# Kernel tuning notes

Hardware: AMD Instinct MI355X
Metric: run time of the kernel (lower is better)

## Reference

```python
import jax, jax.numpy as jnp
import numpy as np

N_NODES = 50000


def _gcn_norm(edge_index, num_nodes):
    # add self loops, compute symmetric normalization D^-1/2 (A+I) D^-1/2
    loops = jnp.arange(num_nodes, dtype=edge_index.dtype)
    row = jnp.concatenate([edge_index[0], loops])
    col = jnp.concatenate([edge_index[1], loops])
    deg = jax.ops.segment_sum(jnp.ones_like(row, dtype=jnp.float32), col,
                              num_segments=num_nodes)
    dinv = jnp.where(deg > 0, jax.lax.rsqrt(deg), 0.0)
    norm = dinv[row] * dinv[col]  # [E']
    return row, col, norm


def _gcn_conv(x, W, b, row, col, norm, num_nodes):
    h = x @ W                       # [N, out] transform first (smaller dim)
    msg = h[row] * norm[:, None]    # gather along source nodes  [E', out]
    agg = jax.ops.segment_sum(msg, col, num_segments=num_nodes)  # scatter-add
    return agg + b


def setup_inputs() -> dict:
    key = jax.random.key(0)
    k1, k2, k3, k4 = jax.random.split(key, 4)
    x = jax.random.normal(k1, (N_NODES, 128), dtype=jnp.float32)
    edge_index = jax.random.randint(k2, (2, 800000), 0, N_NODES, dtype=jnp.int64)
    W1 = jax.random.normal(k3, (128, 128), dtype=jnp.float32) * (1.0 / np.sqrt(128))
    b1 = jnp.zeros((128,), dtype=jnp.float32)
    W2 = jax.random.normal(k4, (128, 16), dtype=jnp.float32) * (1.0 / np.sqrt(128))
    b2 = jnp.zeros((16,), dtype=jnp.float32)
    return {"x": x, "edge_index": edge_index, "W1": W1, "b1": b1, "W2": W2, "b2": b2}


def reference(x, edge_index, W1, b1, W2, b2):
    n = x.shape[0]
    row, col, norm = _gcn_norm(edge_index, n)
    h = _gcn_conv(x, W1, b1, row, col, norm, n)
    h = jax.nn.relu(h)
    h = _gcn_conv(h, W2, b2, row, col, norm, n)
    return jax.nn.log_softmax(h, axis=1)
```

## Files before the change

kernel.cpp:

```cpp
#include <hip/hip_runtime.h>
#include <math.h>

constexpr int N  = 50000;
constexpr int E  = 800000;
constexpr int F1 = 128;
constexpr int F2 = 16;
constexpr int BSHIFT  = 8;
constexpr int NBUCKET = (N + 255) >> BSHIFT;
constexpr int CHUNK   = 2048;
constexpr int CAP     = 6144;
constexpr int SBLK    = (E + CHUNK - 1) / CHUNK;
constexpr int GBLK    = 391;
constexpr int CSTRIDE = 32;

typedef unsigned short ushort_t;
typedef unsigned char  uchar_t;
typedef __bf16 bf16x8 __attribute__((ext_vector_type(8)));
typedef float  f32x4  __attribute__((ext_vector_type(4)));

static __device__ __forceinline__ float blo(unsigned u) { return __uint_as_float(u << 16); }
static __device__ __forceinline__ float bhi(unsigned u) { return __uint_as_float(u & 0xffff0000u); }
static __device__ __forceinline__ ushort_t to_bf(float f) { __bf16 h = (__bf16)f; return *(ushort_t*)&h; }
static __device__ __forceinline__ uchar_t to_fp8(float f) {
    return (uchar_t)(__builtin_amdgcn_cvt_pk_fp8_f32(f, f, 0, false) & 0xff);
}
template <int S>
static __device__ __forceinline__ float cf8(unsigned u) {
    return __builtin_amdgcn_cvt_f32_fp8(u, S);
}

__global__ __launch_bounds__(256) void k_scatterP_gemm1(const int* __restrict__ row,
                                                        const int* __restrict__ col,
                                                        int* __restrict__ cursor,
                                                        unsigned* __restrict__ P,
                                                        const float* __restrict__ x,
                                                        const float* __restrict__ W1,
                                                        uchar_t* __restrict__ h1q) {
    __shared__ __align__(16) ushort_t Wl[F1 * 136];
    int t = threadIdx.x;

    if (blockIdx.x < SBLK) {
        int* hist = (int*)Wl;
        int* loff = hist + 256;
        int* gst  = loff + 256;
        int* lcur = gst + 256;
        int* wtot = lcur + 256;
        unsigned* eb  = (unsigned*)(wtot + 8);
        uchar_t*  bbk = (uchar_t*)(eb + 2048);
        int base = blockIdx.x * CHUNK;
        int total = min(CHUNK, E - base);
        hist[t] = 0;
        __syncthreads();
        int ce[CHUNK / 256];
#pragma unroll
        for (int i = 0; i < CHUNK / 256; ++i) {
            int e = base + i * 256 + t;
            ce[i] = (e < E) ? col[e] : -1;
            if (ce[i] >= 0) atomicAdd(&hist[ce[i] >> BSHIFT], 1);
        }
        __syncthreads();
        {
            int lane = t & 63, wid = t >> 6;
            int v = hist[t];
            int incl = v;
#pragma unroll
            for (int d = 1; d < 64; d <<= 1) {
                int u = __shfl_up(incl, d, 64);
                if (lane >= d) incl += u;
            }
            if (lane == 63) wtot[wid] = incl;
            __syncthreads();
            int wb = 0;
            for (int w = 0; w < wid; ++w) wb += wtot[w];
            int ex = wb + incl - v;
            loff[t] = ex;
            lcur[t] = ex;
            if (t < NBUCKET) gst[t] = t * CAP + atomicAdd(&cursor[t * CSTRIDE], v);
        }
        __syncthreads();
#pragma unroll
        for (int i = 0; i < CHUNK / 256; ++i) {
            int e = base + i * 256 + t;
            if (ce[i] >= 0) {
                int b = ce[i] >> BSHIFT;
                int pos = atomicAdd(&lcur[b], 1);
                eb[pos]  = ((unsigned)row[e] << BSHIFT) | (unsigned)(ce[i] & 255);
                bbk[pos] = (uchar_t)b;
            }
        }
        __syncthreads();
#pragma unroll
        for (int i = 0; i < CHUNK / 256; ++i) {
            int k = i * 256 + t;
            if (k < total) {
                int b = bbk[k];
                P[gst[b] + (k - loff[b])] = eb[k];
            }
        }
        return;
    }

    int gb = blockIdx.x - SBLK;
    {
        int n = t & 127, kh = t >> 7;
#pragma unroll
        for (int j = 0; j < 8; ++j) {
            int k0 = (kh * 8 + j) * 8;
            bf16x8 w;
#pragma unroll
            for (int i2 = 0; i2 < 8; ++i2) w[i2] = (__bf16)W1[(k0 + i2) * F1 + n];
            *(bf16x8*)&Wl[n * 136 + k0] = w;
        }
    }
    __syncthreads();

    int lane = t & 63, wv = t >> 6;
    int quad = lane >> 4, l15 = lane & 15;
#pragma unroll 1
    for (int tile = gb * 2; tile < gb * 2 + 2; ++tile) {
        int arow = tile * 64 + wv * 16 + l15;
        int rclamp = min(arow, N - 1);
        f32x4 acc[8] = {};
#pragma unroll
        for (int kk = 0; kk < 4; ++kk) {
            int k0 = kk * 32 + quad * 8;
            const float* xp = x + (size_t)rclamp * F1 + k0;
            float4 u0 = *(const float4*)xp;
            float4 u1 = *(const float4*)(xp + 4);
            bf16x8 a;
            a[0] = (__bf16)u0.x; a[1] = (__bf16)u0.y; a[2] = (__bf16)u0.z; a[3] = (__bf16)u0.w;
            a[4] = (__bf16)u1.x; a[5] = (__bf16)u1.y; a[6] = (__bf16)u1.z; a[7] = (__bf16)u1.w;
#pragma unroll
            for (int ct = 0; ct < 8; ++ct) {
                bf16x8 b = *(const bf16x8*)&Wl[(ct * 16 + l15) * 136 + k0];
                acc[ct] = __builtin_amdgcn_mfma_f32_16x16x32_bf16(a, b, acc[ct], 0, 0, 0);
            }
        }
        int orow0 = tile * 64 + wv * 16 + quad * 4;
#pragma unroll
        for (int r = 0; r < 4; ++r) {
            int orow = orow0 + r;
            if (orow < N) {
#pragma unroll
                for (int ct = 0; ct < 8; ++ct)
                    h1q[(size_t)orow * F1 + ct * 16 + l15] = to_fp8(acc[ct][r]);
            }
        }
    }
}

__global__ __launch_bounds__(1024) void k_binFinal(const unsigned* __restrict__ P,
                                                   const int* __restrict__ cursor,
                                                   ushort_t* __restrict__ csr16,
                                                   int* __restrict__ seg_start,
                                                   int* __restrict__ counts,
                                                   float* __restrict__ dinv) {
    __shared__ unsigned eb[CAP];
    __shared__ int cnt[256];
    __shared__ int cur[256];
    __shared__ int wtot[4];
    int t = threadIdx.x;
    int b = blockIdx.x;
    int lo = b << BSHIFT;
    int n_nodes = min(256, N - lo);
    int m = cursor[b * CSTRIDE];
    if (t < 256) cnt[t] = 0;
    __syncthreads();
    const unsigned* Pb = P + (size_t)b * CAP;
    for (int k = t; k < m; k += 1024) {
        unsigned u = Pb[k];
        eb[k] = u;
        atomicAdd(&cnt[u & 255], 1);
    }
    __syncthreads();
    int lane = t & 63, wid = t >> 6;
    int v = 0, incl = 0;
    if (t < 256) {
        v = cnt[t];
        incl = v;
#pragma unroll
        for (int d = 1; d < 64; d <<= 1) {
            int u = __shfl_up(incl, d, 64);
            if (lane >= d) incl += u;
        }
        if (lane == 63) wtot[wid] = incl;
    }
    __syncthreads();
    if (t < 256) {
        int wb = 0;
        for (int w = 0; w < wid; ++w) wb += wtot[w];
        int o = b * CAP + wb + incl - v;
        cur[t] = o;
        if (t < n_nodes) {
            seg_start[lo + t] = o;
            counts[lo + t] = v;
            dinv[lo + t] = rsqrtf((float)v + 1.f);
        }
    }
    __syncthreads();
    for (int k = t; k < m; k += 1024) {
        unsigned u = eb[k];
        int pos = atomicAdd(&cur[u & 255], 1);
        csr16[pos] = (ushort_t)(u >> BSHIFT);
    }
}

__global__ __launch_bounds__(256) void k_gather1_gemm2(const uchar_t* __restrict__ h1q,
                                                       const int* __restrict__ seg_start,
                                                       const int* __restrict__ counts,
                                                       const ushort_t* __restrict__ csr16,
                                                       const float* __restrict__ dinv,
                                                       const float* __restrict__ W2,
                                                       const float* __restrict__ b1,
                                                       ushort_t* __restrict__ h2s) {
    __shared__ __align__(16) ushort_t W2l[F2 * 136];
    __shared__ __align__(16) ushort_t T[16 * 136];
    __shared__ float dv[16];
    int t = threadIdx.x;
    for (int i = t; i < F1 * F2; i += 256) {
        int k = i >> 4, n = i & 15;
        W2l[n * 136 + k] = to_bf(W2[i]);
    }
    int lane = t & 63, wv = t >> 6;
    int g = lane >> 4, l15 = lane & 15;
    int gbase = lane & 48;
    int nl = wv * 4 + g;
    int c = blockIdx.x * 16 + nl;
    int cl = min(c, N - 1);

    float dc = 0.f;
    int s = seg_start[cl];
    int cnt = 0;
    if (c < N) { dc = dinv[c]; cnt = counts[c]; }
    uint2 wsf = *(const uint2*)(h1q + ((size_t)cl << 7) + (l15 << 3));
    float4 bL = ((const float4*)b1)[l15 * 2];
    float4 bH = ((const float4*)b1)[l15 * 2 + 1];
    int mcnt = cnt;
    mcnt = max(mcnt, __shfl_xor(mcnt, 16));
    mcnt = max(mcnt, __shfl_xor(mcnt, 32));

    float a0 = 0.f, a1 = 0.f, a2 = 0.f, a3 = 0.f;
    float a4 = 0.f, a5 = 0.f, a6 = 0.f, a7 = 0.f;

#define G1FLT(j_, jb_) { unsigned u = __shfl(pk, gbase + (jb_) + (j_));                     \
        e##j_ = __uint_as_float(u & 0xffff0000u);                                           \
        w##j_ = *(const uint2*)(h1q + ((size_t)(u & 0xffffu) << 7) + (l15 << 3)); }
#define G1ACC(j_) {                                                                         \
        a0 = fmaf(e##j_, cf8<0>(w##j_.x), a0); a1 = fmaf(e##j_, cf8<1>(w##j_.x), a1);       \
        a2 = fmaf(e##j_, cf8<2>(w##j_.x), a2); a3 = fmaf(e##j_, cf8<3>(w##j_.x), a3);       \
        a4 = fmaf(e##j_, cf8<0>(w##j_.y), a4); a5 = fmaf(e##j_, cf8<1>(w##j_.y), a5);       \
        a6 = fmaf(e##j_, cf8<2>(w##j_.y), a6); a7 = fmaf(e##j_, cf8<3>(w##j_.y), a7); }

    unsigned pk = 0;
    {   int k = l15;
        if (k < cnt) {
            int r = csr16[s + k];
            pk = ((unsigned)to_bf(dinv[r]) << 16) | (unsigned)r;
        }
    }
#pragma unroll 1
    for (int k0 = 0; k0 < mcnt; k0 += 16) {
        unsigned pknext = 0;
        {   int k = k0 + 16 + l15;
            if (k < cnt) {
                int r = csr16[s + k];
                pknext = ((unsigned)to_bf(dinv[r]) << 16) | (unsigned)r;
            }
        }
        {
            uint2 w0, w1, w2, w3, w4, w5, w6, w7;
            float e0, e1, e2, e3, e4, e5, e6, e7;
            G1FLT(0, 0) G1FLT(1, 0) G1FLT(2, 0) G1FLT(3, 0)
            G1FLT(4, 0) G1FLT(5, 0) G1FLT(6, 0) G1FLT(7, 0)
            G1ACC(0) G1ACC(1) G1ACC(2) G1ACC(3)
            G1ACC(4) G1ACC(5) G1ACC(6) G1ACC(7)
        }
        if (k0 + 8 < mcnt) {
            uint2 w0, w1, w2, w3, w4, w5, w6, w7;
            float e0, e1, e2, e3, e4, e5, e6, e7;
            G1FLT(0, 8) G1FLT(1, 8) G1FLT(2, 8) G1FLT(3, 8)
            G1FLT(4, 8) G1FLT(5, 8) G1FLT(6, 8) G1FLT(7, 8)
            G1ACC(0) G1ACC(1) G1ACC(2) G1ACC(3)
            G1ACC(4) G1ACC(5) G1ACC(6) G1ACC(7)
        }
        pk = pknext;
    }
#undef G1FLT
#undef G1ACC

    {
        a0 = fmaf(dc, cf8<0>(wsf.x), a0); a1 = fmaf(dc, cf8<1>(wsf.x), a1);
        a2 = fmaf(dc, cf8<2>(wsf.x), a2); a3 = fmaf(dc, cf8<3>(wsf.x), a3);
        a4 = fmaf(dc, cf8<0>(wsf.y), a4); a5 = fmaf(dc, cf8<1>(wsf.y), a5);
        a6 = fmaf(dc, cf8<2>(wsf.y), a6); a7 = fmaf(dc, cf8<3>(wsf.y), a7);
        a0 = fmaxf(fmaf(dc, a0, bL.x), 0.f); a1 = fmaxf(fmaf(dc, a1, bL.y), 0.f);
        a2 = fmaxf(fmaf(dc, a2, bL.z), 0.f); a3 = fmaxf(fmaf(dc, a3, bL.w), 0.f);
        a4 = fmaxf(fmaf(dc, a4, bH.x), 0.f); a5 = fmaxf(fmaf(dc, a5, bH.y), 0.f);
        a6 = fmaxf(fmaf(dc, a6, bH.z), 0.f); a7 = fmaxf(fmaf(dc, a7, bH.w), 0.f);
        uint4 pp;
        pp.x = (unsigned)to_bf(a0) | ((unsigned)to_bf(a1) << 16);
        pp.y = (unsigned)to_bf(a2) | ((unsigned)to_bf(a3) << 16);
        pp.z = (unsigned)to_bf(a4) | ((unsigned)to_bf(a5) << 16);
        pp.w = (unsigned)to_bf(a6) | ((unsigned)to_bf(a7) << 16);
        *(uint4*)&T[nl * 136 + (l15 << 3)] = pp;
        if (l15 == 0) dv[nl] = dc;
    }
    __syncthreads();

    if (wv == 0) {
        int quad = lane >> 4;
        f32x4 acc = {};
#pragma unroll
        for (int kk = 0; kk < 4; ++kk) {
            int k0 = kk * 32 + quad * 8;
            bf16x8 a = *(const bf16x8*)&T[l15 * 136 + k0];
            bf16x8 b = *(const bf16x8*)&W2l[l15 * 136 + k0];
            acc = __builtin_amdgcn_mfma_f32_16x16x32_bf16(a, b, acc, 0, 0, 0);
        }
#pragma unroll
        for (int r = 0; r < 4; ++r) {
            int rw = quad * 4 + r;
            int gn = blockIdx.x * 16 + rw;
            if (gn < N) h2s[(size_t)gn * F2 + l15] = to_bf(acc[r] * dv[rw]);
        }
    }
}

__global__ __launch_bounds__(256) void k_gather2(const ushort_t* __restrict__ h2s,
                                                 const int* __restrict__ seg_start,
                                                 const int* __restrict__ counts,
                                                 const ushort_t* __restrict__ csr16,
                                                 const float* __restrict__ dinv,
                                                 const float* __restrict__ b2,
                                                 float* __restrict__ out) {
    int idx = blockIdx.x * 256 + threadIdx.x;
    int node = idx >> 3, sub = idx & 7;
    if (node >= N) return;
    int lane = threadIdx.x & 63;
    int gb = lane & 56;
    int s = seg_start[node], cntc = counts[node];
    float dc = dinv[node];
    float2 bb = ((const float2*)b2)[sub];
    unsigned us = ((const unsigned*)(h2s + (size_t)node * F2))[sub];
    float ax = 0.f, ay = 0.f;

#define G2LOAD(n_) { int src = gb | min(n_, rem - 1); int r = __shfl(rl, src);              \
        w##n_ = ((const unsigned*)(h2s + (size_t)r * F2))[sub]; if (n_ >= rem) w##n_ = 0u; }

    int rl = 0;
    if (sub < min(cntc, 8)) rl = csr16[s + sub];
#pragma unroll 1
    for (int j0 = 0; j0 < cntc; j0 += 8) {
        int rem = min(cntc - j0, 8);
        int rlnext = 0;
        int j2 = j0 + 8;
        if (j2 < cntc && sub < cntc - j2) rlnext = csr16[s + j2 + sub];
        unsigned w0, w1, w2, w3, w4, w5, w6, w7;
        G2LOAD(0) G2LOAD(1) G2LOAD(2) G2LOAD(3)
        G2LOAD(4) G2LOAD(5) G2LOAD(6) G2LOAD(7)
        ax += ((blo(w0) + blo(w1)) + (blo(w2) + blo(w3))) +
              ((blo(w4) + blo(w5)) + (blo(w6) + blo(w7)));
        ay += ((bhi(w0) + bhi(w1)) + (bhi(w2) + bhi(w3))) +
              ((bhi(w4) + bhi(w5)) + (bhi(w6) + bhi(w7)));
        rl = rlnext;
    }
#undef G2LOAD
    ax += blo(us);
    ay += bhi(us);
    float v0 = fmaf(dc, ax, bb.x);
    float v1 = fmaf(dc, ay, bb.y);
    float mx = fmaxf(v0, v1);
#pragma unroll
    for (int m = 1; m < 8; m <<= 1) mx = fmaxf(mx, __shfl_xor(mx, m));
    float sm = expf(v0 - mx) + expf(v1 - mx);
#pragma unroll
    for (int m = 1; m < 8; m <<= 1) sm += __shfl_xor(sm, m);
    float lse = mx + logf(sm);
    float2 o;
    o.x = v0 - lse;
    o.y = v1 - lse;
    ((float2*)(out + (size_t)node * F2))[sub] = o;
}

extern "C" void kernel_launch(void* const* d_in, const int* in_sizes, int n_in,
                              void* d_out, int out_size, void* d_ws, size_t ws_size,
                              hipStream_t stream) {
    const float* x  = (const float*)d_in[0];
    const int*   ei = (const int*)d_in[1];
    const float* W1 = (const float*)d_in[2];
    const float* b1 = (const float*)d_in[3];
    const float* W2 = (const float*)d_in[4];
    const float* b2 = (const float*)d_in[5];
    const int* row = ei;
    const int* col = ei + E;

    char* ws = (char*)d_ws;
    int*      cursor    = (int*)ws;      ws += 256 * CSTRIDE * 4;
    unsigned* P         = (unsigned*)ws; ws += (size_t)NBUCKET * CAP * 4;
    ushort_t* csr16     = (ushort_t*)ws; ws += (size_t)NBUCKET * CAP * 2;
    int*      seg_start = (int*)ws;      ws += (size_t)N * 4;
    int*      counts    = (int*)ws;      ws += (size_t)N * 4;
    float*    dinv      = (float*)ws;    ws += (size_t)N * 4;
    uchar_t*  h1q       = (uchar_t*)ws;  ws += (size_t)N * F1;
    ushort_t* h2s       = (ushort_t*)ws; ws += (size_t)N * F2 * 2;

    (void)hipMemsetAsync(cursor, 0, 256 * CSTRIDE * 4, stream);

    k_scatterP_gemm1<<<SBLK + GBLK, 256, 0, stream>>>(row, col, cursor, P, x, W1, h1q);
    k_binFinal<<<NBUCKET, 1024, 0, stream>>>(P, cursor, csr16, seg_start, counts, dinv);
    k_gather1_gemm2<<<(N + 15) / 16, 256, 0, stream>>>(h1q, seg_start, counts, csr16,
                                                       dinv, W2, b1, h2s);
    k_gather2<<<((size_t)N * 8 + 255) / 256, 256, 0, stream>>>(h2s, seg_start, counts, csr16,
                                                               dinv, b2, (float*)d_out);
}
```

Baseline: 142.7 us.

## Fuse all four stages into one cooperative persistent kernel with grid syncs

Replaces the memset and four separate launches with a single cooperative kernel sized from occupancy, using grid.sync between the scatter/GEMM1, bucket-finalize, gather1/GEMM2 and gather2 phases. The bucket scatter no longer uses global atomic cursors. Each chunk writes its locally sorted edges plus per-bucket counts and offsets, and the finalize phase rebuilds each bucket with a scan and a binary search. This removes launch gaps and global atomics, but adds grid-wide barriers and a persistent-loop schedule that may underuse the GPU in some phases, since finalize runs on only 196 blocks.

```diff
diff --git a/kernel.cpp b/kernel.cpp
--- a/kernel.cpp
+++ b/kernel.cpp
@@ -1,5 +1,8 @@
 #include <hip/hip_runtime.h>
+#include <hip/hip_cooperative_groups.h>
 #include <math.h>
+
+namespace cg = cooperative_groups;
 
 constexpr int N  = 50000;
 constexpr int E  = 800000;
@@ -10,8 +13,8 @@
 constexpr int CHUNK   = 2048;
 constexpr int CAP     = 6144;
 constexpr int SBLK    = (E + CHUNK - 1) / CHUNK;
-constexpr int GBLK    = 391;
-constexpr int CSTRIDE = 32;
+constexpr int TILES   = (N + 63) / 64;
+constexpr int GTILES  = (N + 15) / 16;
 
 typedef unsigned short ushort_t;
 typedef unsigned char  uchar_t;
@@ -29,218 +32,202 @@
     return __builtin_amdgcn_cvt_f32_fp8(u, S);
 }
 
-__global__ __launch_bounds__(256) void k_scatterP_gemm1(const int* __restrict__ row,
-                                                        const int* __restrict__ col,
-                                                        int* __restrict__ cursor,
-                                                        unsigned* __restrict__ P,
-                                                        const float* __restrict__ x,
-                                                        const float* __restrict__ W1,
-                                                        uchar_t* __restrict__ h1q) {
-    __shared__ __align__(16) ushort_t Wl[F1 * 136];
+static __device__ __forceinline__ int excl_scan256(int v, int* wtot, int& tot) {
     int t = threadIdx.x;
-
-    if (blockIdx.x < SBLK) {
-        int* hist = (int*)Wl;
+    int lane = t & 63, wid = t >> 6;
+    int incl = v;
+#pragma unroll
+    for (int d = 1; d < 64; d <<= 1) {
+        int u = __shfl_up(incl, d, 64);
+        if (lane >= d) incl += u;
+    }
+    if (lane == 63) wtot[wid] = incl;
+    __syncthreads();
+    int wb = 0;
+    for (int w = 0; w < wid; ++w) wb += wtot[w];
+    tot = wtot[0] + wtot[1] + wtot[2] + wtot[3];
+    __syncthreads();
+    return wb + incl - v;
+}
+
+__global__ __launch_bounds__(256, 4) void k_mega(
+    const int* __restrict__ row, const int* __restrict__ col,
+    const float* __restrict__ x, const float* __restrict__ W1,
+    const float* __restrict__ b1, const float* __restrict__ W2,
+    const float* __restrict__ b2,
+    unsigned* __restrict__ P2, int* __restrict__ cnt_g, int* __restrict__ loff_g,
+    ushort_t* __restrict__ csr16, int* __restrict__ seg_start,
+    int* __restrict__ counts, float* __restrict__ dinv,
+    uchar_t* __restrict__ h1q, ushort_t* __restrict__ h2s,
+    float* __restrict__ out)
+{
+    __shared__ __align__(16) char smem[35072];
+    cg::grid_group grid = cg::this_grid();
+    int t   = threadIdx.x;
+    int NBk = (int)gridDim.x;
+
+    int SC = min(SBLK, max(1, (NBk * 2) / 5));
+    if ((int)blockIdx.x < SC) {
+        int* hist = (int*)smem;
         int* loff = hist + 256;
-        int* gst  = loff + 256;
-        int* lcur = gst + 256;
+        int* lcur = loff + 256;
         int* wtot = lcur + 256;
-        unsigned* eb  = (unsigned*)(wtot + 8);
-        uchar_t*  bbk = (uchar_t*)(eb + 2048);
-        int base = blockIdx.x * CHUNK;
-        int total = min(CHUNK, E - base);
-        hist[t] = 0;
-        __syncthreads();
-        int ce[CHUNK / 256];
-#pragma unroll
-        for (int i = 0; i < CHUNK / 256; ++i) {
-            int e = base + i * 256 + t;
-            ce[i] = (e < E) ? col[e] : -1;
-            if (ce[i] >= 0) atomicAdd(&hist[ce[i] >> BSHIFT], 1);
-        }
-        __syncthreads();
-        {
-            int lane = t & 63, wid = t >> 6;
-            int v = hist[t];
-            int incl = v;
-#pragma unroll
-            for (int d = 1; d < 64; d <<= 1) {
-                int u = __shfl_up(incl, d, 64);
-                if (lane >= d) incl += u;
-            }
-            if (lane == 63) wtot[wid] = incl;
-            __syncthreads();
-            int wb = 0;
-            for (int w = 0; w < wid; ++w) wb += wtot[w];
-            int ex = wb + incl - v;
+        unsigned* eb = (unsigned*)(wtot + 8);
+        for (int j = blockIdx.x; j < SBLK; j += SC) {
+            hist[t] = 0;
+            __syncthreads();
+            int base = j * CHUNK;
+            int ce[CHUNK / 256];
+#pragma unroll
+            for (int i = 0; i < CHUNK / 256; ++i) {
+                int e = base + i * 256 + t;
+                ce[i] = (e < E) ? col[e] : -1;
+                if (ce[i] >= 0) atomicAdd(&hist[ce[i] >> BSHIFT], 1);
+            }
+            __syncthreads();
+            int tot;
+            int ex = excl_scan256(hist[t], wtot, tot);
             loff[t] = ex;
             lcur[t] = ex;
-            if (t < NBUCKET) gst[t] = t * CAP + atomicAdd(&cursor[t * CSTRIDE], v);
+            if (t < NBUCKET) { cnt_g[t * SBLK + j] = hist[t]; loff_g[t * SBLK + j] = ex; }
+            __syncthreads();
+#pragma unroll
+            for (int i = 0; i < CHUNK / 256; ++i) {
+                int e = base + i * 256 + t;
+                if (ce[i] >= 0) {
+                    int pos = atomicAdd(&lcur[ce[i] >> BSHIFT], 1);
+                    eb[pos] = ((unsigned)row[e] << BSHIFT) | (unsigned)(ce[i] & 255);
+                }
+            }
+            __syncthreads();
+            int total = min(CHUNK, E - base);
+#pragma unroll
+            for (int i = 0; i < CHUNK / 256; ++i) {
+                int k = i * 256 + t;
+                if (k < total) P2[base + k] = eb[k];
+            }
+            __syncthreads();
+        }
+    } else {
+        ushort_t* Wl = (ushort_t*)smem;
+        {
+            int n = t & 127, kh = t >> 7;
+#pragma unroll
+            for (int j = 0; j < 8; ++j) {
+                int k0 = (kh * 8 + j) * 8;
+                bf16x8 w;
+#pragma unroll
+                for (int i2 = 0; i2 < 8; ++i2) w[i2] = (__bf16)W1[(k0 + i2) * F1 + n];
+                *(bf16x8*)&Wl[n * 136 + k0] = w;
+            }
         }
         __syncthreads();
-#pragma unroll
-        for (int i = 0; i < CHUNK / 256; ++i) {
-            int e = base + i * 256 + t;
-            if (ce[i] >= 0) {
-                int b = ce[i] >> BSHIFT;
-                int pos = atomicAdd(&lcur[b], 1);
-                eb[pos]  = ((unsigned)row[e] << BSHIFT) | (unsigned)(ce[i] & 255);
-                bbk[pos] = (uchar_t)b;
-            }
-        }
+        int lane = t & 63, wv = t >> 6;
+        int quad = lane >> 4, l15 = lane & 15;
+        int gcount = NBk - SC;
+#pragma unroll 1
+        for (int tile = (int)blockIdx.x - SC; tile < TILES; tile += gcount) {
+            int arow = tile * 64 + wv * 16 + l15;
+            int rclamp = min(arow, N - 1);
+            f32x4 acc[8] = {};
+#pragma unroll
+            for (int kk = 0; kk < 4; ++kk) {
+                int k0 = kk * 32 + quad * 8;
+                const float* xp = x + (size_t)rclamp * F1 + k0;
+                float4 u0 = *(const float4*)xp;
+                float4 u1 = *(const float4*)(xp + 4);
+                bf16x8 a;
+                a[0] = (__bf16)u0.x; a[1] = (__bf16)u0.y; a[2] = (__bf16)u0.z; a[3] = (__bf16)u0.w;
+                a[4] = (__bf16)u1.x; a[5] = (__bf16)u1.y; a[6] = (__bf16)u1.z; a[7] = (__bf16)u1.w;
+#pragma unroll
+                for (int ct = 0; ct < 8; ++ct) {
+                    bf16x8 bfr = *(const bf16x8*)&Wl[(ct * 16 + l15) * 136 + k0];
+                    acc[ct] = __builtin_amdgcn_mfma_f32_16x16x32_bf16(a, bfr, acc[ct], 0, 0, 0);
+                }
+            }
+            int orow0 = tile * 64 + wv * 16 + quad * 4;
+#pragma unroll
+            for (int r = 0; r < 4; ++r) {
+                int orow = orow0 + r;
+                if (orow < N) {
+#pragma unroll
+                    for (int ct = 0; ct < 8; ++ct)
+                        h1q[(size_t)orow * F1 + ct * 16 + l15] = to_fp8(acc[ct][r]);
+                }
+            }
+        }
+    }
+    __threadfence();
+    grid.sync();
+
+    if ((int)blockIdx.x < NBUCKET) {
+        int b = blockIdx.x;
+        int* cS    = (int*)smem;
+        int* oS    = cS + SBLK;
+        int* baseS = oS + SBLK;
+        int* wtot2 = baseS + 392;
+        int* cnt   = wtot2 + 8;
+        int* cur   = cnt + 256;
+        unsigned* eb2 = (unsigned*)(cur + 256);
+        for (int jj = t; jj < SBLK; jj += 256) {
+            cS[jj] = cnt_g[b * SBLK + jj];
+            oS[jj] = loff_g[b * SBLK + jj];
+        }
+        cnt[t] = 0;
         __syncthreads();
-#pragma unroll
-        for (int i = 0; i < CHUNK / 256; ++i) {
-            int k = i * 256 + t;
-            if (k < total) {
-                int b = bbk[k];
-                P[gst[b] + (k - loff[b])] = eb[k];
-            }
-        }
-        return;
-    }
-
-    int gb = blockIdx.x - SBLK;
+        int tot0 = 0, tot1 = 0;
+        int e0 = excl_scan256(cS[t], wtot2, tot0);
+        baseS[t] = e0;
+        int v1 = (256 + t < SBLK) ? cS[256 + t] : 0;
+        int e1 = excl_scan256(v1, wtot2, tot1);
+        if (256 + t < SBLK) baseS[256 + t] = tot0 + e1;
+        int m = tot0 + tot1;
+        __syncthreads();
+        for (int k = t; k < m; k += 256) {
+            int lo2 = 0, hi2 = SBLK - 1;
+            while (lo2 < hi2) {
+                int mid = (lo2 + hi2 + 1) >> 1;
+                if (baseS[mid] <= k) lo2 = mid; else hi2 = mid - 1;
+            }
+            unsigned u = P2[lo2 * CHUNK + oS[lo2] + (k - baseS[lo2])];
+            eb2[k] = u;
+            atomicAdd(&cnt[u & 255], 1);
+        }
+        __syncthreads();
+        int tot2;
+        int exn = excl_scan256(cnt[t], wtot2, tot2);
+        int o = b * CAP + exn;
+        cur[t] = o;
+        int lo = b << BSHIFT;
+        int myc = cnt[t];
+        if (lo + t < N) {
+            seg_start[lo + t] = o;
+            counts[lo + t]    = myc;
+            dinv[lo + t]      = rsqrtf((float)myc + 1.f);
+        }
+        __syncthreads();
+        for (int k = t; k < m; k += 256) {
+            unsigned u = eb2[k];
+            int pos = atomicAdd(&cur[u & 255], 1);
+            csr16[pos] = (ushort_t)(u >> BSHIFT);
+        }
+    }
+    __threadfence();
+    grid.sync();
+
     {
-        int n = t & 127, kh = t >> 7;
-#pragma unroll
-        for (int j = 0; j < 8; ++j) {
-            int k0 = (kh * 8 + j) * 8;
-            bf16x8 w;
-#pragma unroll
-            for (int i2 = 0; i2 < 8; ++i2) w[i2] = (__bf16)W1[(k0 + i2) * F1 + n];
-            *(bf16x8*)&Wl[n * 136 + k0] = w;
-        }
-    }
-    __syncthreads();
-
-    int lane = t & 63, wv = t >> 6;
-    int quad = lane >> 4, l15 = lane & 15;
-#pragma unroll 1
-    for (int tile = gb * 2; tile < gb * 2 + 2; ++tile) {
-        int arow = tile * 64 + wv * 16 + l15;
-        int rclamp = min(arow, N - 1);
-        f32x4 acc[8] = {};
-#pragma unroll
-        for (int kk = 0; kk < 4; ++kk) {
-            int k0 = kk * 32 + quad * 8;
-            const float* xp = x + (size_t)rclamp * F1 + k0;
-            float4 u0 = *(const float4*)xp;
-            float4 u1 = *(const float4*)(xp + 4);
-            bf16x8 a;
-            a[0] = (__bf16)u0.x; a[1] = (__bf16)u0.y; a[2] = (__bf16)u0.z; a[3] = (__bf16)u0.w;
-            a[4] = (__bf16)u1.x; a[5] = (__bf16)u1.y; a[6] = (__bf16)u1.z; a[7] = (__bf16)u1.w;
-#pragma unroll
-            for (int ct = 0; ct < 8; ++ct) {
-                bf16x8 b = *(const bf16x8*)&Wl[(ct * 16 + l15) * 136 + k0];
-                acc[ct] = __builtin_amdgcn_mfma_f32_16x16x32_bf16(a, b, acc[ct], 0, 0, 0);
-            }
-        }
-        int orow0 = tile * 64 + wv * 16 + quad * 4;
-#pragma unroll
-        for (int r = 0; r < 4; ++r) {
-            int orow = orow0 + r;
-            if (orow < N) {
-#pragma unroll
-                for (int ct = 0; ct < 8; ++ct)
-                    h1q[(size_t)orow * F1 + ct * 16 + l15] = to_fp8(acc[ct][r]);
-            }
-        }
-    }
-}
-
-__global__ __launch_bounds__(1024) void k_binFinal(const unsigned* __restrict__ P,
-                                                   const int* __restrict__ cursor,
-                                                   ushort_t* __restrict__ csr16,
-                                                   int* __restrict__ seg_start,
-                                                   int* __restrict__ counts,
-                                                   float* __restrict__ dinv) {
-    __shared__ unsigned eb[CAP];
-    __shared__ int cnt[256];
-    __shared__ int cur[256];
-    __shared__ int wtot[4];
-    int t = threadIdx.x;
-    int b = blockIdx.x;
-    int lo = b << BSHIFT;
-    int n_nodes = min(256, N - lo);
-    int m = cursor[b * CSTRIDE];
-    if (t < 256) cnt[t] = 0;
-    __syncthreads();
-    const unsigned* Pb = P + (size_t)b * CAP;
-    for (int k = t; k < m; k += 1024) {
-        unsigned u = Pb[k];
-        eb[k] = u;
-        atomicAdd(&cnt[u & 255], 1);
-    }
-    __syncthreads();
-    int lane = t & 63, wid = t >> 6;
-    int v = 0, incl = 0;
-    if (t < 256) {
-        v = cnt[t];
-        incl = v;
-#pragma unroll
-        for (int d = 1; d < 64; d <<= 1) {
-            int u = __shfl_up(incl, d, 64);
-            if (lane >= d) incl += u;
-        }
-        if (lane == 63) wtot[wid] = incl;
-    }
-    __syncthreads();
-    if (t < 256) {
-        int wb = 0;
-        for (int w = 0; w < wid; ++w) wb += wtot[w];
-        int o = b * CAP + wb + incl - v;
-        cur[t] = o;
-        if (t < n_nodes) {
-            seg_start[lo + t] = o;
-            counts[lo + t] = v;
-            dinv[lo + t] = rsqrtf((float)v + 1.f);
-        }
-    }
-    __syncthreads();
-    for (int k = t; k < m; k += 1024) {
-        unsigned u = eb[k];
-        int pos = atomicAdd(&cur[u & 255], 1);
-        csr16[pos] = (ushort_t)(u >> BSHIFT);
-    }
-}
-
-__global__ __launch_bounds__(256) void k_gather1_gemm2(const uchar_t* __restrict__ h1q,
-                                                       const int* __restrict__ seg_start,
-                                                       const int* __restrict__ counts,
-                                                       const ushort_t* __restrict__ csr16,
-                                                       const float* __restrict__ dinv,
-                                                       const float* __restrict__ W2,
-                                                       const float* __restrict__ b1,
-                                                       ushort_t* __restrict__ h2s) {
-    __shared__ __align__(16) ushort_t W2l[F2 * 136];
-    __shared__ __align__(16) ushort_t T[16 * 136];
-    __shared__ float dv[16];
-    int t = threadIdx.x;
-    for (int i = t; i < F1 * F2; i += 256) {
-        int k = i >> 4, n = i & 15;
-        W2l[n * 136 + k] = to_bf(W2[i]);
-    }
-    int lane = t & 63, wv = t >> 6;
-    int g = lane >> 4, l15 = lane & 15;
-    int gbase = lane & 48;
-    int nl = wv * 4 + g;
-    int c = blockIdx.x * 16 + nl;
-    int cl = min(c, N - 1);
-
-    float dc = 0.f;
-    int s = seg_start[cl];
-    int cnt = 0;
-    if (c < N) { dc = dinv[c]; cnt = counts[c]; }
-    uint2 wsf = *(const uint2*)(h1q + ((size_t)cl << 7) + (l15 << 3));
-    float4 bL = ((const float4*)b1)[l15 * 2];
-    float4 bH = ((const float4*)b1)[l15 * 2 + 1];
-    int mcnt = cnt;
-    mcnt = max(mcnt, __shfl_xor(mcnt, 16));
-    mcnt = max(mcnt, __shfl_xor(mcnt, 32));
-
-    float a0 = 0.f, a1 = 0.f, a2 = 0.f, a3 = 0.f;
-    float a4 = 0.f, a5 = 0.f, a6 = 0.f, a7 = 0.f;
+        ushort_t* W2l = (ushort_t*)smem;
+        ushort_t* T   = W2l + F2 * 136;
+        float*    dv  = (float*)(T + 16 * 136);
+        for (int i = t; i < F1 * F2; i += 256) {
+            int k = i >> 4, n = i & 15;
+            W2l[n * 136 + k] = to_bf(W2[i]);
+        }
+        int lane = t & 63, wv = t >> 6;
+        int g = lane >> 4, l15 = lane & 15;
+        int gbase = lane & 48;
+        float4 bL = ((const float4*)b1)[l15 * 2];
+        float4 bH = ((const float4*)b1)[l15 * 2 + 1];
 
 #define G1FLT(j_, jb_) { unsigned u = __shfl(pk, gbase + (jb_) + (j_));                     \
         e##j_ = __uint_as_float(u & 0xffff0000u);                                           \
@@ -251,135 +238,151 @@
         a4 = fmaf(e##j_, cf8<0>(w##j_.y), a4); a5 = fmaf(e##j_, cf8<1>(w##j_.y), a5);       \
         a6 = fmaf(e##j_, cf8<2>(w##j_.y), a6); a7 = fmaf(e##j_, cf8<3>(w##j_.y), a7); }
 
-    unsigned pk = 0;
-    {   int k = l15;
-        if (k < cnt) {
-            int r = csr16[s + k];
-            pk = ((unsigned)to_bf(dinv[r]) << 16) | (unsigned)r;
-        }
-    }
 #pragma unroll 1
-    for (int k0 = 0; k0 < mcnt; k0 += 16) {
-        unsigned pknext = 0;
-        {   int k = k0 + 16 + l15;
-            if (k < cnt) {
-                int r = csr16[s + k];
-                pknext = ((unsigned)to_bf(dinv[r]) << 16) | (unsigned)r;
-            }
-        }
-        {
-            uint2 w0, w1, w2, w3, w4, w5, w6, w7;
-            float e0, e1, e2, e3, e4, e5, e6, e7;
-            G1FLT(0, 0) G1FLT(1, 0) G1FLT(2, 0) G1FLT(3, 0)
-            G1FLT(4, 0) G1FLT(5, 0) G1FLT(6, 0) G1FLT(7, 0)
-            G1ACC(0) G1ACC(1) G1ACC(2) G1ACC(3)
-            G1ACC(4) G1ACC(5) G1ACC(6) G1ACC(7)
-        }
-        if (k0 + 8 < mcnt) {
-            uint2 w0, w1, w2, w3, w4, w5, w6, w7;
-            float e0, e1, e2, e3, e4, e5, e6, e7;
-            G1FLT(0, 8) G1FLT(1, 8) G1FLT(2, 8) G1FLT(3, 8)
-            G1FLT(4, 8) G1FLT(5, 8) G1FLT(6, 8) G1FLT(7, 8)
-            G1ACC(0) G1ACC(1) G1ACC(2) G1ACC(3)
-            G1ACC(4) G1ACC(5) G1ACC(6) G1ACC(7)
-        }
-        pk = pknext;
-    }
+        for (int tile = blockIdx.x; tile < GTILES; tile += NBk) {
+            __syncthreads();
+            int nl = wv * 4 + g;
+            int c = tile * 16 + nl;
+            int cl = min(c, N - 1);
+            float dc = 0.f;
+            int s = seg_start[cl];
+            int cnt3 = 0;
+            if (c < N) { dc = dinv[c]; cnt3 = counts[c]; }
+            uint2 wsf = *(const uint2*)(h1q + ((size_t)cl << 7) + (l15 << 3));
+            int mcnt = cnt3;
+            mcnt = max(mcnt, __shfl_xor(mcnt, 16));
+            mcnt = max(mcnt, __shfl_xor(mcnt, 32));
+
+            float a0 = 0.f, a1 = 0.f, a2 = 0.f, a3 = 0.f;
+            float a4 = 0.f, a5 = 0.f, a6 = 0.f, a7 = 0.f;
+            unsigned pk = 0;
+            {
+                int k = l15;
+                if (k < cnt3) {
+                    int r = csr16[s + k];
+                    pk = ((unsigned)to_bf(dinv[r]) << 16) | (unsigned)r;
+                }
+            }
+#pragma unroll 1
+            for (int k0 = 0; k0 < mcnt; k0 += 16) {
+                unsigned pknext = 0;
+                {
+                    int k = k0 + 16 + l15;
+                    if (k < cnt3) {
+                        int r = csr16[s + k];
+                        pknext = ((unsigned)to_bf(dinv[r]) << 16) | (unsigned)r;
+                    }
+                }
+                {
+                    uint2 w0, w1, w2, w3, w4, w5, w6, w7;
+                    float e0, e1, e2, e3, e4, e5, e6, e7;
+                    G1FLT(0, 0) G1FLT(1, 0) G1FLT(2, 0) G1FLT(3, 0)
+                    G1FLT(4, 0) G1FLT(5, 0) G1FLT(6, 0) G1FLT(7, 0)
+                    G1ACC(0) G1ACC(1) G1ACC(2) G1ACC(3)
+                    G1ACC(4) G1ACC(5) G1ACC(6) G1ACC(7)
+                }
+                if (k0 + 8 < mcnt) {
+                    uint2 w0, w1, w2, w3, w4, w5, w6, w7;
+                    float e0, e1, e2, e3, e4, e5, e6, e7;
+                    G1FLT(0, 8) G1FLT(1, 8) G1FLT(2, 8) G1FLT(3, 8)
+                    G1FLT(4, 8) G1FLT(5, 8) G1FLT(6, 8) G1FLT(7, 8)
+                    G1ACC(0) G1ACC(1) G1ACC(2) G1ACC(3)
+                    G1ACC(4) G1ACC(5) G1ACC(6) G1ACC(7)
+                }
+                pk = pknext;
+            }
+            {
+                a0 = fmaf(dc, cf8<0>(wsf.x), a0); a1 = fmaf(dc, cf8<1>(wsf.x), a1);
+                a2 = fmaf(dc, cf8<2>(wsf.x), a2); a3 = fmaf(dc, cf8<3>(wsf.x), a3);
+                a4 = fmaf(dc, cf8<0>(wsf.y), a4); a5 = fmaf(dc, cf8<1>(wsf.y), a5);
+                a6 = fmaf(dc, cf8<2>(wsf.y), a6); a7 = fmaf(dc, cf8<3>(wsf.y), a7);
+                a0 = fmaxf(fmaf(dc, a0, bL.x), 0.f); a1 = fmaxf(fmaf(dc, a1, bL.y), 0.f);
+                a2 = fmaxf(fmaf(dc, a2, bL.z), 0.f); a3 = fmaxf(fmaf(dc, a3, bL.w), 0.f);
+                a4 = fmaxf(fmaf(dc, a4, bH.x), 0.f); a5 = fmaxf(fmaf(dc, a5, bH.y), 0.f);
+                a6 = fmaxf(fmaf(dc, a6, bH.z), 0.f); a7 = fmaxf(fmaf(dc, a7, bH.w), 0.f);
+                uint4 pp;
+                pp.x = (unsigned)to_bf(a0) | ((unsigned)to_bf(a1) << 16);
+                pp.y = (unsigned)to_bf(a2) | ((unsigned)to_bf(a3) << 16);
+                pp.z = (unsigned)to_bf(a4) | ((unsigned)to_bf(a5) << 16);
+                pp.w = (unsigned)to_bf(a6) | ((unsigned)to_bf(a7) << 16);
+                *(uint4*)&T[nl * 136 + (l15 << 3)] = pp;
+                if (l15 == 0) dv[nl] = dc;
+            }
+            __syncthreads();
+            if (wv == 0) {
+                int quad = lane >> 4;
+                f32x4 acc = {};
+#pragma unroll
+                for (int kk = 0; kk < 4; ++kk) {
+                    int k0 = kk * 32 + quad * 8;
+                    bf16x8 a = *(const bf16x8*)&T[l15 * 136 + k0];
+                    bf16x8 bfr = *(const bf16x8*)&W2l[l15 * 136 + k0];
+                    acc = __builtin_amdgcn_mfma_f32_16x16x32_bf16(a, bfr, acc, 0, 0, 0);
+                }
+#pragma unroll
+                for (int r = 0; r < 4; ++r) {
+                    int rw = quad * 4 + r;
+                    int gn = tile * 16 + rw;
+                    if (gn < N) h2s[(size_t)gn * F2 + l15] = to_bf(acc[r] * dv[rw]);
+                }
+            }
+        }
 #undef G1FLT
 #undef G1ACC
+    }
+    __threadfence();
+    grid.sync();
 
     {
-        a0 = fmaf(dc, cf8<0>(wsf.x), a0); a1 = fmaf(dc, cf8<1>(wsf.x), a1);
-        a2 = fmaf(dc, cf8<2>(wsf.x), a2); a3 = fmaf(dc, cf8<3>(wsf.x), a3);
-        a4 = fmaf(dc, cf8<0>(wsf.y), a4); a5 = fmaf(dc, cf8<1>(wsf.y), a5);
-        a6 = fmaf(dc, cf8<2>(wsf.y), a6); a7 = fmaf(dc, cf8<3>(wsf.y), a7);
-        a0 = fmaxf(fmaf(dc, a0, bL.x), 0.f); a1 = fmaxf(fmaf(dc, a1, bL.y), 0.f);
-        a2 = fmaxf(fmaf(dc, a2, bL.z), 0.f); a3 = fmaxf(fmaf(dc, a3, bL.w), 0.f);
-        a4 = fmaxf(fmaf(dc, a4, bH.x), 0.f); a5 = fmaxf(fmaf(dc, a5, bH.y), 0.f);
-        a6 = fmaxf(fmaf(dc, a6, bH.z), 0.f); a7 = fmaxf(fmaf(dc, a7, bH.w), 0.f);
-        uint4 pp;
-        pp.x = (unsigned)to_bf(a0) | ((unsigned)to_bf(a1) << 16);
-        pp.y = (unsigned)to_bf(a2) | ((unsigned)to_bf(a3) << 16);
-        pp.z = (unsigned)to_bf(a4) | ((unsigned)to_bf(a5) << 16);
-        pp.w = (unsigned)to_bf(a6) | ((unsigned)to_bf(a7) << 16);
-        *(uint4*)&T[nl * 136 + (l15 << 3)] = pp;
-        if (l15 == 0) dv[nl] = dc;
-    }
-    __syncthreads();
-
-    if (wv == 0) {
-        int quad = lane >> 4;
-        f32x4 acc = {};
-#pragma unroll
-        for (int kk = 0; kk < 4; ++kk) {
-            int k0 = kk * 32 + quad * 8;
-            bf16x8 a = *(const bf16x8*)&T[l15 * 136 + k0];
-            bf16x8 b = *(const bf16x8*)&W2l[l15 * 136 + k0];
-            acc = __builtin_amdgcn_mfma_f32_16x16x32_bf16(a, b, acc, 0, 0, 0);
-        }
-#pragma unroll
-        for (int r = 0; r < 4; ++r) {
-            int rw = quad * 4 + r;
-            int gn = blockIdx.x * 16 + rw;
-            if (gn < N) h2s[(size_t)gn * F2 + l15] = to_bf(acc[r] * dv[rw]);
-        }
-    }
-}
-
-__global__ __launch_bounds__(256) void k_gather2(const ushort_t* __restrict__ h2s,
-                                                 const int* __restrict__ seg_start,
-                                                 const int* __restrict__ counts,
-                                                 const ushort_t* __restrict__ csr16,
-                                                 const float* __restrict__ dinv,
-                                                 const float* __restrict__ b2,
-                                                 float* __restrict__ out) {
-    int idx = blockIdx.x * 256 + threadIdx.x;
-    int node = idx >> 3, sub = idx & 7;
-    if (node >= N) return;
-    int lane = threadIdx.x & 63;
-    int gb = lane & 56;
-    int s = seg_start[node], cntc = counts[node];
-    float dc = dinv[node];
-    float2 bb = ((const float2*)b2)[sub];
-    unsigned us = ((const unsigned*)(h2s + (size_t)node * F2))[sub];
-    float ax = 0.f, ay = 0.f;
+        int lane = t & 63;
+        int gb = lane & 56;
+#pragma unroll 1
+        for (int idx = (int)blockIdx.x * 256 + t; idx < N * 8; idx += NBk * 256) {
+            int node = idx >> 3, sub = idx & 7;
+            int s = seg_start[node], cntc = counts[node];
+            float dc = dinv[node];
+            float2 bb = ((const float2*)b2)[sub];
+            unsigned us = ((const unsigned*)(h2s + (size_t)node * F2))[sub];
+            float ax = 0.f, ay = 0.f;
 
 #define G2LOAD(n_) { int src = gb | min(n_, rem - 1); int r = __shfl(rl, src);              \
         w##n_ = ((const unsigned*)(h2s + (size_t)r * F2))[sub]; if (n_ >= rem) w##n_ = 0u; }
 
-    int rl = 0;
-    if (sub < min(cntc, 8)) rl = csr16[s + sub];
+            int rl = 0;
+            if (sub < min(cntc, 8)) rl = csr16[s + sub];
 #pragma unroll 1
-    for (int j0 = 0; j0 < cntc; j0 += 8) {
-        int rem = min(cntc - j0, 8);
-        int rlnext = 0;
-        int j2 = j0 + 8;
-        if (j2 < cntc && sub < cntc - j2) rlnext = csr16[s + j2 + sub];
-        unsigned w0, w1, w2, w3, w4, w5, w6, w7;
-        G2LOAD(0) G2LOAD(1) G2LOAD(2) G2LOAD(3)
-        G2LOAD(4) G2LOAD(5) G2LOAD(6) G2LOAD(7)
-        ax += ((blo(w0) + blo(w1)) + (blo(w2) + blo(w3))) +
-              ((blo(w4) + blo(w5)) + (blo(w6) + blo(w7)));
-        ay += ((bhi(w0) + bhi(w1)) + (bhi(w2) + bhi(w3))) +
-              ((bhi(w4) + bhi(w5)) + (bhi(w6) + bhi(w7)));
-        rl = rlnext;
-    }
+            for (int j0 = 0; j0 < cntc; j0 += 8) {
+                int rem = min(cntc - j0, 8);
+                int rlnext = 0;
+                int j2 = j0 + 8;
+                if (j2 < cntc && sub < cntc - j2) rlnext = csr16[s + j2 + sub];
+                unsigned w0, w1, w2, w3, w4, w5, w6, w7;
+                G2LOAD(0) G2LOAD(1) G2LOAD(2) G2LOAD(3)
+                G2LOAD(4) G2LOAD(5) G2LOAD(6) G2LOAD(7)
+                ax += ((blo(w0) + blo(w1)) + (blo(w2) + blo(w3))) +
+                      ((blo(w4) + blo(w5)) + (blo(w6) + blo(w7)));
+                ay += ((bhi(w0) + bhi(w1)) + (bhi(w2) + bhi(w3))) +
+                      ((bhi(w4) + bhi(w5)) + (bhi(w6) + bhi(w7)));
+                rl = rlnext;
+            }
 #undef G2LOAD
-    ax += blo(us);
-    ay += bhi(us);
-    float v0 = fmaf(dc, ax, bb.x);
-    float v1 = fmaf(dc, ay, bb.y);
-    float mx = fmaxf(v0, v1);
-#pragma unroll
-    for (int m = 1; m < 8; m <<= 1) mx = fmaxf(mx, __shfl_xor(mx, m));
-    float sm = expf(v0 - mx) + expf(v1 - mx);
-#pragma unroll
-    for (int m = 1; m < 8; m <<= 1) sm += __shfl_xor(sm, m);
-    float lse = mx + logf(sm);
-    float2 o;
-    o.x = v0 - lse;
-    o.y = v1 - lse;
-    ((float2*)(out + (size_t)node * F2))[sub] = o;
+            ax += blo(us);
+            ay += bhi(us);
+            float v0 = fmaf(dc, ax, bb.x);
+            float v1 = fmaf(dc, ay, bb.y);
+            float mx = fmaxf(v0, v1);
+#pragma unroll
+            for (int mm = 1; mm < 8; mm <<= 1) mx = fmaxf(mx, __shfl_xor(mx, mm));
+            float sm = expf(v0 - mx) + expf(v1 - mx);
+#pragma unroll
+            for (int mm = 1; mm < 8; mm <<= 1) sm += __shfl_xor(sm, mm);
+            float lse = mx + logf(sm);
+            float2 o;
+            o.x = v0 - lse;
+            o.y = v1 - lse;
+            ((float2*)(out + (size_t)node * F2))[sub] = o;
+        }
+    }
 }
 
 extern "C" void kernel_launch(void* const* d_in, const int* in_sizes, int n_in,
@@ -391,25 +394,35 @@
     const float* b1 = (const float*)d_in[3];
     const float* W2 = (const float*)d_in[4];
     const float* b2 = (const float*)d_in[5];
-    const int* row = ei;
-    const int* col = ei + E;
+    const int* rowp = ei;
+    const int* colp = ei + E;
 
     char* ws = (char*)d_ws;
-    int*      cursor    = (int*)ws;      ws += 256 * CSTRIDE * 4;
-    unsigned* P         = (unsigned*)ws; ws += (size_t)NBUCKET * CAP * 4;
+    unsigned* P2        = (unsigned*)ws; ws += (size_t)SBLK * CHUNK * 4;
+    int*      cnt_g     = (int*)ws;      ws += (size_t)NBUCKET * SBLK * 4;
+    int*      loff_g    = (int*)ws;      ws += (size_t)NBUCKET * SBLK * 4;
     ushort_t* csr16     = (ushort_t*)ws; ws += (size_t)NBUCKET * CAP * 2;
     int*      seg_start = (int*)ws;      ws += (size_t)N * 4;
     int*      counts    = (int*)ws;      ws += (size_t)N * 4;
-    float*    dinv      = (float*)ws;    ws += (size_t)N * 4;
+    float*    dinvp     = (float*)ws;    ws += (size_t)N * 4;
     uchar_t*  h1q       = (uchar_t*)ws;  ws += (size_t)N * F1;
     ushort_t* h2s       = (ushort_t*)ws; ws += (size_t)N * F2 * 2;
-
-    (void)hipMemsetAsync(cursor, 0, 256 * CSTRIDE * 4, stream);
-
-    k_scatterP_gemm1<<<SBLK + GBLK, 256, 0, stream>>>(row, col, cursor, P, x, W1, h1q);
-    k_binFinal<<<NBUCKET, 1024, 0, stream>>>(P, cursor, csr16, seg_start, counts, dinv);
-    k_gather1_gemm2<<<(N + 15) / 16, 256, 0, stream>>>(h1q, seg_start, counts, csr16,
-                                                       dinv, W2, b1, h2s);
-    k_gather2<<<((size_t)N * 8 + 255) / 256, 256, 0, stream>>>(h2s, seg_start, counts, csr16,
-                                                               dinv, b2, (float*)d_out);
+    float*    outp      = (float*)d_out;
+
+    static int NB = 0;
+    if (NB == 0) {
+        int mbs = 0;
+        (void)hipOccupancyMaxActiveBlocksPerMultiprocessor(&mbs, k_mega, 256, 0);
+        if (mbs < 1) mbs = 1;
+        long nb = (long)mbs * 256;
+        NB = (int)(nb > 1024 ? 1024 : nb);
+        if (NB < 256) NB = 256;
+    }
+
+    void* args[] = { (void*)&rowp, (void*)&colp, (void*)&x, (void*)&W1, (void*)&b1,
+                     (void*)&W2, (void*)&b2, (void*)&P2, (void*)&cnt_g, (void*)&loff_g,
+                     (void*)&csr16, (void*)&seg_start, (void*)&counts, (void*)&dinvp,
+                     (void*)&h1q, (void*)&h2s, (void*)&outp };
+    (void)hipLaunchCooperativeKernel((const void*)k_mega, dim3(NB), dim3(256),
+                                     args, 0, stream);
 }
```

Result: slower. 529.5 us (+271.0%).

## Replace global-atomic bucket scatter with per-chunk sorted runs and offset tables

Applied to the files above, without the earlier changes.

The edge-bucketing pass now writes each chunk's locally bucket-sorted edges contiguously to global memory and records per-(bucket,chunk) counts and offsets, instead of claiming slots with global atomics and scattering. The binning kernel scans the per-chunk counts for its bucket and gathers its edges from every chunk via binary search over prefix offsets. This removes the memset and the global atomic contention and makes the writes coalesced, at the cost of scattered reads and a binary search per edge in the second kernel, which also drops from 1024 to 512 threads.

```diff
diff --git a/kernel.cpp b/kernel.cpp
--- a/kernel.cpp
+++ b/kernel.cpp
@@ -11,7 +11,6 @@
 constexpr int CAP     = 6144;
 constexpr int SBLK    = (E + CHUNK - 1) / CHUNK;
 constexpr int GBLK    = 391;
-constexpr int CSTRIDE = 32;
 
 typedef unsigned short ushort_t;
 typedef unsigned char  uchar_t;
@@ -31,24 +30,22 @@
 
 __global__ __launch_bounds__(256) void k_scatterP_gemm1(const int* __restrict__ row,
                                                         const int* __restrict__ col,
-                                                        int* __restrict__ cursor,
-                                                        unsigned* __restrict__ P,
+                                                        unsigned* __restrict__ P2,
+                                                        int* __restrict__ cnt_g,
+                                                        int* __restrict__ loff_g,
                                                         const float* __restrict__ x,
                                                         const float* __restrict__ W1,
                                                         uchar_t* __restrict__ h1q) {
-    __shared__ __align__(16) ushort_t Wl[F1 * 136];
+    __shared__ __align__(16) char smem[F1 * 136 * 2];
     int t = threadIdx.x;
 
     if (blockIdx.x < SBLK) {
-        int* hist = (int*)Wl;
-        int* loff = hist + 256;
-        int* gst  = loff + 256;
-        int* lcur = gst + 256;
+        int* hist = (int*)smem;
+        int* lcur = hist + 256;
         int* wtot = lcur + 256;
-        unsigned* eb  = (unsigned*)(wtot + 8);
-        uchar_t*  bbk = (uchar_t*)(eb + 2048);
-        int base = blockIdx.x * CHUNK;
-        int total = min(CHUNK, E - base);
+        unsigned* eb = (unsigned*)(wtot + 8);
+        int j = blockIdx.x;
+        int base = j * CHUNK;
         hist[t] = 0;
         __syncthreads();
         int ce[CHUNK / 256];
@@ -73,33 +70,29 @@
             int wb = 0;
             for (int w = 0; w < wid; ++w) wb += wtot[w];
             int ex = wb + incl - v;
-            loff[t] = ex;
             lcur[t] = ex;
-            if (t < NBUCKET) gst[t] = t * CAP + atomicAdd(&cursor[t * CSTRIDE], v);
+            if (t < NBUCKET) { cnt_g[t * SBLK + j] = v; loff_g[t * SBLK + j] = ex; }
         }
         __syncthreads();
 #pragma unroll
         for (int i = 0; i < CHUNK / 256; ++i) {
             int e = base + i * 256 + t;
             if (ce[i] >= 0) {
-                int b = ce[i] >> BSHIFT;
-                int pos = atomicAdd(&lcur[b], 1);
-                eb[pos]  = ((unsigned)row[e] << BSHIFT) | (unsigned)(ce[i] & 255);
-                bbk[pos] = (uchar_t)b;
-            }
-        }
-        __syncthreads();
+                int pos = atomicAdd(&lcur[ce[i] >> BSHIFT], 1);
+                eb[pos] = ((unsigned)row[e] << BSHIFT) | (unsigned)(ce[i] & 255);
+            }
+        }
+        __syncthreads();
+        int total = min(CHUNK, E - base);
 #pragma unroll
         for (int i = 0; i < CHUNK / 256; ++i) {
             int k = i * 256 + t;
-            if (k < total) {
-                int b = bbk[k];
-                P[gst[b] + (k - loff[b])] = eb[k];
-            }
+            if (k < total) P2[base + k] = eb[k];
         }
         return;
     }
 
+    ushort_t* Wl = (ushort_t*)smem;
     int gb = blockIdx.x - SBLK;
     {
         int n = t & 127, kh = t >> 7;
@@ -132,8 +125,8 @@
             a[4] = (__bf16)u1.x; a[5] = (__bf16)u1.y; a[6] = (__bf16)u1.z; a[7] = (__bf16)u1.w;
 #pragma unroll
             for (int ct = 0; ct < 8; ++ct) {
-                bf16x8 b = *(const bf16x8*)&Wl[(ct * 16 + l15) * 136 + k0];
-                acc[ct] = __builtin_amdgcn_mfma_f32_16x16x32_bf16(a, b, acc[ct], 0, 0, 0);
+                bf16x8 bfr = *(const bf16x8*)&Wl[(ct * 16 + l15) * 136 + k0];
+                acc[ct] = __builtin_amdgcn_mfma_f32_16x16x32_bf16(a, bfr, acc[ct], 0, 0, 0);
             }
         }
         int orow0 = tile * 64 + wv * 16 + quad * 4;
@@ -149,57 +142,83 @@
     }
 }
 
-__global__ __launch_bounds__(1024) void k_binFinal(const unsigned* __restrict__ P,
-                                                   const int* __restrict__ cursor,
-                                                   ushort_t* __restrict__ csr16,
-                                                   int* __restrict__ seg_start,
-                                                   int* __restrict__ counts,
-                                                   float* __restrict__ dinv) {
-    __shared__ unsigned eb[CAP];
+__global__ __launch_bounds__(512) void k_binFinal(const unsigned* __restrict__ P2,
+                                                  const int* __restrict__ cnt_g,
+                                                  const int* __restrict__ loff_g,
+                                                  ushort_t* __restrict__ csr16,
+                                                  int* __restrict__ seg_start,
+                                                  int* __restrict__ counts,
+                                                  float* __restrict__ dinv) {
+    __shared__ int cS[SBLK];
+    __shared__ int oS[SBLK];
+    __shared__ int baseS[SBLK];
+    __shared__ int wtot[8];
     __shared__ int cnt[256];
     __shared__ int cur[256];
-    __shared__ int wtot[4];
+    __shared__ unsigned eb2[CAP];
     int t = threadIdx.x;
     int b = blockIdx.x;
     int lo = b << BSHIFT;
-    int n_nodes = min(256, N - lo);
-    int m = cursor[b * CSTRIDE];
+    if (t < SBLK) { cS[t] = cnt_g[b * SBLK + t]; oS[t] = loff_g[b * SBLK + t]; }
     if (t < 256) cnt[t] = 0;
     __syncthreads();
-    const unsigned* Pb = P + (size_t)b * CAP;
-    for (int k = t; k < m; k += 1024) {
-        unsigned u = Pb[k];
-        eb[k] = u;
-        atomicAdd(&cnt[u & 255], 1);
-    }
-    __syncthreads();
-    int lane = t & 63, wid = t >> 6;
-    int v = 0, incl = 0;
-    if (t < 256) {
-        v = cnt[t];
-        incl = v;
+    int m;
+    {
+        int lane = t & 63, wid = t >> 6;
+        int v = (t < SBLK) ? cS[t] : 0;
+        int incl = v;
 #pragma unroll
         for (int d = 1; d < 64; d <<= 1) {
             int u = __shfl_up(incl, d, 64);
             if (lane >= d) incl += u;
         }
         if (lane == 63) wtot[wid] = incl;
-    }
-    __syncthreads();
-    if (t < 256) {
+        __syncthreads();
         int wb = 0;
         for (int w = 0; w < wid; ++w) wb += wtot[w];
-        int o = b * CAP + wb + incl - v;
-        cur[t] = o;
-        if (t < n_nodes) {
-            seg_start[lo + t] = o;
-            counts[lo + t] = v;
-            dinv[lo + t] = rsqrtf((float)v + 1.f);
-        }
-    }
-    __syncthreads();
-    for (int k = t; k < m; k += 1024) {
-        unsigned u = eb[k];
+        m = 0;
+#pragma unroll
+        for (int w = 0; w < 8; ++w) m += wtot[w];
+        if (t < SBLK) baseS[t] = wb + incl - v;
+    }
+    __syncthreads();
+    for (int k = t; k < m; k += 512) {
+        int lo2 = 0, hi2 = SBLK - 1;
+        while (lo2 < hi2) {
+            int mid = (lo2 + hi2 + 1) >> 1;
+            if (baseS[mid] <= k) lo2 = mid; else hi2 = mid - 1;
+        }
+        unsigned u = P2[lo2 * CHUNK + oS[lo2] + (k - baseS[lo2])];
+        eb2[k] = u;
+        atomicAdd(&cnt[u & 255], 1);
+    }
+    __syncthreads();
+    {
+        int lane = t & 63, wid = t >> 6;
+        int v = (t < 256) ? cnt[t] : 0;
+        int incl = v;
+#pragma unroll
+        for (int d = 1; d < 64; d <<= 1) {
+            int u = __shfl_up(incl, d, 64);
+            if (lane >= d) incl += u;
+        }
+        if (lane == 63) wtot[wid] = incl;
+        __syncthreads();
+        int wb = 0;
+        for (int w = 0; w < wid; ++w) wb += wtot[w];
+        if (t < 256) {
+            int o = b * CAP + wb + incl - v;
+            cur[t] = o;
+            if (lo + t < N) {
+                seg_start[lo + t] = o;
+                counts[lo + t]    = v;
+                dinv[lo + t]      = rsqrtf((float)v + 1.f);
+            }
+        }
+    }
+    __syncthreads();
+    for (int k = t; k < m; k += 512) {
+        unsigned u = eb2[k];
         int pos = atomicAdd(&cur[u & 255], 1);
         csr16[pos] = (ushort_t)(u >> BSHIFT);
     }
@@ -314,8 +333,8 @@
         for (int kk = 0; kk < 4; ++kk) {
             int k0 = kk * 32 + quad * 8;
             bf16x8 a = *(const bf16x8*)&T[l15 * 136 + k0];
-            bf16x8 b = *(const bf16x8*)&W2l[l15 * 136 + k0];
-            acc = __builtin_amdgcn_mfma_f32_16x16x32_bf16(a, b, acc, 0, 0, 0);
+            bf16x8 bfr = *(const bf16x8*)&W2l[l15 * 136 + k0];
+            acc = __builtin_amdgcn_mfma_f32_16x16x32_bf16(a, bfr, acc, 0, 0, 0);
         }
 #pragma unroll
         for (int r = 0; r < 4; ++r) {
@@ -391,25 +410,26 @@
     const float* b1 = (const float*)d_in[3];
     const float* W2 = (const float*)d_in[4];
     const float* b2 = (const float*)d_in[5];
-    const int* row = ei;
-    const int* col = ei + E;
+    const int* rowp = ei;
+    const int* colp = ei + E;
 
     char* ws = (char*)d_ws;
-    int*      cursor    = (int*)ws;      ws += 256 * CSTRIDE * 4;
-    unsigned* P         = (unsigned*)ws; ws += (size_t)NBUCKET * CAP * 4;
+    unsigned* P2        = (unsigned*)ws; ws += (size_t)SBLK * CHUNK * 4;
+    int*      cnt_g     = (int*)ws;      ws += (size_t)NBUCKET * SBLK * 4;
+    int*      loff_g    = (int*)ws;      ws += (size_t)NBUCKET * SBLK * 4;
     ushort_t* csr16     = (ushort_t*)ws; ws += (size_t)NBUCKET * CAP * 2;
     int*      seg_start = (int*)ws;      ws += (size_t)N * 4;
     int*      counts    = (int*)ws;      ws += (size_t)N * 4;
-    float*    dinv      = (float*)ws;    ws += (size_t)N * 4;
+    float*    dinvp     = (float*)ws;    ws += (size_t)N * 4;
     uchar_t*  h1q       = (uchar_t*)ws;  ws += (size_t)N * F1;
     ushort_t* h2s       = (ushort_t*)ws; ws += (size_t)N * F2 * 2;
 
-    (void)hipMemsetAsync(cursor, 0, 256 * CSTRIDE * 4, stream);
-
-    k_scatterP_gemm1<<<SBLK + GBLK, 256, 0, stream>>>(row, col, cursor, P, x, W1, h1q);
-    k_binFinal<<<NBUCKET, 1024, 0, stream>>>(P, cursor, csr16, seg_start, counts, dinv);
+    k_scatterP_gemm1<<<SBLK + GBLK, 256, 0, stream>>>(rowp, colp, P2, cnt_g, loff_g,
+                                                      x, W1, h1q);
+    k_binFinal<<<NBUCKET, 512, 0, stream>>>(P2, cnt_g, loff_g, csr16, seg_start,
+                                            counts, dinvp);
     k_gather1_gemm2<<<(N + 15) / 16, 256, 0, stream>>>(h1q, seg_start, counts, csr16,
-                                                       dinv, W2, b1, h2s);
+                                                       dinvp, W2, b1, h2s);
     k_gather2<<<((size_t)N * 8 + 255) / 256, 256, 0, stream>>>(h2s, seg_start, counts, csr16,
-                                                               dinv, b2, (float*)d_out);
-}
+                                                               dinvp, b2, (float*)d_out);
+}
```

Measured after the change: 145.6 us. +2.0%, slower.
